# Kernel optimization log

Measured on AMD Instinct MI355X. Metric: run time of the kernel, lower is better.

## Reference

```python
import jax, jax.numpy as jnp
import numpy as np

EPS = 1e-6

def setup_inputs() -> dict:
    key = jax.random.key(0)
    k1, k2, k3 = jax.random.split(key, 3)
    B, N, C = 128, 196, 1024  # B = b*f = 8*16
    x = jax.random.normal(k1, (B, N, C), dtype=jnp.float32)
    w_qkv = jax.random.normal(k2, (3 * C, C), dtype=jnp.float32) * (C ** -0.5)
    w_proj = jax.random.normal(k3, (C, C), dtype=jnp.float32) * (C ** -0.5)
    b_proj = jnp.zeros((C,), dtype=jnp.float32)
    return {"x": x, "w_qkv": w_qkv, "w_proj": w_proj, "b_proj": b_proj, "num_frames": 16}

def reference(x, w_qkv, w_proj, b_proj, num_frames):
    B, N, C = x.shape
    H = 16
    e = C // H
    scale = e ** -0.5
    f = num_frames
    b = B // f
    # qkv projection (no bias), split k-first per rearrange 'b n (k c) -> k b n c'
    qkv = jnp.einsum('bnc,dc->bnd', x, w_qkv)          # [B, N, 3C]
    qkv = qkv.reshape(B, N, 3, H, e)
    q, k, v = qkv[:, :, 0], qkv[:, :, 1], qkv[:, :, 2]  # [B, N, H, e]
    # relu feature map + scale offset
    q_ = jax.nn.relu(q) + scale
    k_ = jax.nn.relu(k) + scale
    # fold frames into the token axis per video: [b, f*n, H, e]
    L = f * N
    q_ = q_.reshape(b, L, H, e)
    k_ = k_.reshape(b, L, H, e)
    v_ = v.reshape(b, L, H, e)
    # linear attention: kv accumulation [b, H, e, e]
    kv = jnp.einsum('bnhe,bnhd->bhed', k_, v_)
    k_sum = jnp.sum(k_, axis=1, keepdims=True)          # [b, 1, H, e]
    z = 1.0 / (jnp.sum(q_ * k_sum, axis=-1) + EPS)       # [b, L, H]
    out = jnp.einsum('bnhe,bhed->bnhd', q_, kv) * z[..., None]  # [b, L, H, e]
    out = out.reshape(B, N, C)
    return jnp.einsum('bnc,dc->bnd', out, w_proj) + b_proj
```

## Files before the change

### kernel.cpp

```cpp
#include <hip/hip_runtime.h>
#include <hip/hip_bf16.h>
#include <stdint.h>

typedef __attribute__((ext_vector_type(8))) short bf16x8;
typedef __attribute__((ext_vector_type(4))) float f32x4;

__device__ __forceinline__ unsigned short f2bf(float f) {
    unsigned u = __builtin_bit_cast(unsigned, f);
    u += 0x7FFF + ((u >> 16) & 1);
    return (unsigned short)(u >> 16);
}
__device__ __forceinline__ float bf2f(unsigned short h) {
    return __builtin_bit_cast(float, (unsigned)h << 16);
}
__device__ __forceinline__ void load_lds16(const void* g, void* l) {
    __builtin_amdgcn_global_load_lds(
        (const __attribute__((address_space(1))) void*)g,
        (__attribute__((address_space(3))) void*)l, 16, 0, 0);
}

__global__ __launch_bounds__(256)
void cvt_kernel(const float* __restrict__ src, unsigned short* __restrict__ dst)
{
    const long i = ((long)blockIdx.x * 256 + threadIdx.x) * 8;
    const float4 a = *(const float4*)(src + i);
    const float4 b = *(const float4*)(src + i + 4);
    bf16x8 r;
    r[0] = (short)f2bf(a.x); r[1] = (short)f2bf(a.y);
    r[2] = (short)f2bf(a.z); r[3] = (short)f2bf(a.w);
    r[4] = (short)f2bf(b.x); r[5] = (short)f2bf(b.y);
    r[6] = (short)f2bf(b.z); r[7] = (short)f2bf(b.w);
    *(bf16x8*)(dst + i) = r;
}

#define LD_A(p, i, s) (*(const bf16x8*)&lds[p][wr][((i) * 16 + fr) * 64 + ((((s) << 2) + qd) ^ cx) * 8])
#define LD_B(p, j, s) (*(const bf16x8*)&lds[p][2 + bh_][(brow_ + (j) * 16 + fr) * 64 + ((((s) << 2) + qd) ^ cx) * 8])

#define LDA4(p, ib) do { \
    afr[0][0] = LD_A(p, (ib)+0, 0); afr[0][1] = LD_A(p, (ib)+0, 1); \
    afr[1][0] = LD_A(p, (ib)+1, 0); afr[1][1] = LD_A(p, (ib)+1, 1); \
    afr[2][0] = LD_A(p, (ib)+2, 0); afr[2][1] = LD_A(p, (ib)+2, 1); \
    afr[3][0] = LD_A(p, (ib)+3, 0); afr[3][1] = LD_A(p, (ib)+3, 1); \
} while (0)

#define LDB2(p, jb) do { \
    bfr[(jb)+0][0] = LD_B(p, (jb)+0, 0); bfr[(jb)+0][1] = LD_B(p, (jb)+0, 1); \
    bfr[(jb)+1][0] = LD_B(p, (jb)+1, 0); bfr[(jb)+1][1] = LD_B(p, (jb)+1, 1); \
} while (0)

#define STAGE_A(p, half, tile) do { \
    const unsigned short* s_ = Ag + (long)((half) * 128) * 1024 + (tile) * 64; \
    unsigned short* d_ = ldsw + ((p) * 4 + (half)) * 8192; \
    load_lds16(s_, d_); \
    load_lds16(s_ + (long)64 * 1024, d_ + 4096); \
} while (0)

#define STAGE_B(p, half, tile) do { \
    const unsigned short* s_ = Bg + (long)((half) * 128) * 1024 + (tile) * 64; \
    unsigned short* d_ = ldsw + ((p) * 4 + 2 + (half)) * 8192; \
    load_lds16(s_, d_); \
    load_lds16(s_ + (long)64 * 1024, d_ + 4096); \
} while (0)

#define MM(ib, jb) do { \
    _Pragma("unroll") \
    for (int i_ = 0; i_ < 4; ++i_) { \
        acc[(ib)+i_][(jb)+0] = __builtin_amdgcn_mfma_f32_16x16x32_bf16(afr[i_][0], bfr[(jb)+0][0], acc[(ib)+i_][(jb)+0], 0, 0, 0); \
        acc[(ib)+i_][(jb)+1] = __builtin_amdgcn_mfma_f32_16x16x32_bf16(afr[i_][0], bfr[(jb)+1][0], acc[(ib)+i_][(jb)+1], 0, 0, 0); \
    } \
    _Pragma("unroll") \
    for (int i_ = 0; i_ < 4; ++i_) { \
        acc[(ib)+i_][(jb)+0] = __builtin_amdgcn_mfma_f32_16x16x32_bf16(afr[i_][1], bfr[(jb)+0][1], acc[(ib)+i_][(jb)+0], 0, 0, 0); \
        acc[(ib)+i_][(jb)+1] = __builtin_amdgcn_mfma_f32_16x16x32_bf16(afr[i_][1], bfr[(jb)+1][1], acc[(ib)+i_][(jb)+1], 0, 0, 0); \
    } \
} while (0)

#define PH_MID() do { \
    __builtin_amdgcn_sched_barrier(0); \
    __builtin_amdgcn_s_barrier(); \
    asm volatile("s_waitcnt lgkmcnt(0)" ::: "memory"); \
    __builtin_amdgcn_sched_barrier(0); \
    __builtin_amdgcn_s_setprio(1); \
} while (0)

#define PH_END() do { \
    __builtin_amdgcn_s_setprio(0); \
    __builtin_amdgcn_s_barrier(); \
} while (0)

#define PH_END_V(n) do { \
    __builtin_amdgcn_s_setprio(0); \
    asm volatile("s_waitcnt vmcnt(" #n ")" ::: "memory"); \
    __builtin_amdgcn_s_barrier(); \
} while (0)

template<int MODE>
__global__ __launch_bounds__(512, 2)
void gemm_bt_kernel(const unsigned short* __restrict__ A,
                    const unsigned short* __restrict__ Bt,
                    __hip_bfloat16* __restrict__ o0,
                    __hip_bfloat16* __restrict__ o1,
                    __hip_bfloat16* __restrict__ o2,
                    float* __restrict__ outf,
                    const float* __restrict__ bias)
{
    constexpr int K  = 1024;
    constexpr int NT = (MODE == 0) ? 12 : 4;
    __shared__ __attribute__((aligned(16))) unsigned short lds[2][4][8192];

    const int bid   = blockIdx.x;
    const int npg   = 8 * NT;
    const int group = bid / npg;
    const int rem   = bid - group * npg;
    const int gm    = (98 - group * 8 < 8) ? (98 - group * 8) : 8;
    const int mt    = group * 8 + rem % gm;
    const int nt    = rem / gm;
    const long m0 = (long)mt * 256;
    const long n0 = (long)nt * 256;

    const int t    = threadIdx.x;
    const int lane = t & 63;
    const int wv   = t >> 6;
    const int wr   = wv >> 2;
    const int wc   = wv & 3;
    const int fr   = lane & 15;
    const int qd   = lane >> 4;
    const int cx   = fr & 7;
    const int bh_   = wc >> 1;
    const int brow_ = (wc & 1) << 6;

    const int srow = t >> 3;
    const int gch  = (t & 7) ^ (srow & 7);
    const unsigned short* Ag = A  + (m0 + srow) * K + gch * 8;
    const unsigned short* Bg = Bt + (n0 + srow) * K + gch * 8;
    unsigned short* const ldsw = &lds[0][0][0] + wv * 512;

    f32x4 acc[8][4] = {};
    bf16x8 afr[4][2], bfr[4][2];

    STAGE_B(0, 0, 0); STAGE_B(0, 1, 0); STAGE_A(0, 0, 0); STAGE_A(0, 1, 0);
    STAGE_B(1, 0, 1); STAGE_B(1, 1, 1);
    asm volatile("s_waitcnt vmcnt(4)" ::: "memory");
    __builtin_amdgcn_s_barrier();

#pragma unroll 1
    for (int it = 0; it < 7; ++it) {
        const int t1 = 2 * it + 1, t2 = 2 * it + 2, t3 = 2 * it + 3;
        LDA4(0, 0); LDB2(0, 0); STAGE_A(1, 0, t1);
        PH_MID(); MM(0, 0); PH_END();
        LDB2(0, 2); STAGE_A(1, 1, t1);
        PH_MID(); MM(0, 2); PH_END();
        LDA4(0, 4); STAGE_B(0, 0, t2);
        PH_MID(); MM(4, 0); PH_END();
        STAGE_B(0, 1, t2);
        PH_MID(); MM(4, 2); PH_END_V(4);
        LDA4(1, 0); LDB2(1, 0); STAGE_A(0, 0, t2);
        PH_MID(); MM(0, 0); PH_END();
        LDB2(1, 2); STAGE_A(0, 1, t2);
        PH_MID(); MM(0, 2); PH_END();
        LDA4(1, 4); STAGE_B(1, 0, t3);
        PH_MID(); MM(4, 0); PH_END();
        STAGE_B(1, 1, t3);
        PH_MID(); MM(4, 2); PH_END_V(4);
    }
    LDA4(0, 0); LDB2(0, 0); STAGE_A(1, 0, 15);
    PH_MID(); MM(0, 0); PH_END();
    LDB2(0, 2); STAGE_A(1, 1, 15);
    PH_MID(); MM(0, 2); PH_END();
    LDA4(0, 4);
    PH_MID(); MM(4, 0); PH_END();
    PH_MID(); MM(4, 2); PH_END_V(0);
    LDA4(1, 0); LDB2(1, 0);
    PH_MID(); MM(0, 0); PH_END();
    LDB2(1, 2);
    PH_MID(); MM(0, 2); PH_END();
    LDA4(1, 4);
    PH_MID(); MM(4, 0); PH_END();
    __builtin_amdgcn_s_barrier();
    asm volatile("s_waitcnt lgkmcnt(0)" ::: "memory");
    __builtin_amdgcn_sched_barrier(0);
    __builtin_amdgcn_s_setprio(1); MM(4, 2); __builtin_amdgcn_s_setprio(0);

    if (MODE == 0) {
        const int which = nt >> 2;
        __hip_bfloat16* dst = (which == 0) ? o0 : (which == 1) ? o1 : o2;
        const int colbase = ((nt & 3) << 8) + wc * 64;
        const bool act = (which < 2);
#pragma unroll
        for (int i = 0; i < 8; ++i) {
            const long mrow = m0 + wr * 128 + i * 16 + qd * 4;
#pragma unroll
            for (int r = 0; r < 4; ++r) {
                const long moff = (mrow + r) * 1024;
#pragma unroll
                for (int j = 0; j < 4; ++j) {
                    float v = acc[i][j][r];
                    if (act) v = fmaxf(v, 0.f) + 0.125f;
                    dst[moff + colbase + j * 16 + fr] = __float2bfloat16(v);
                }
            }
        }
    } else {
        const long nbase = n0 + wc * 64;
#pragma unroll
        for (int i = 0; i < 8; ++i) {
            const long mrow = m0 + wr * 128 + i * 16 + qd * 4;
#pragma unroll
            for (int r = 0; r < 4; ++r) {
                const long moff = (mrow + r) * 1024;
#pragma unroll
                for (int j = 0; j < 4; ++j)
                    outf[moff + nbase + j * 16 + fr] =
                        acc[i][j][r] + bias[nbase + j * 16 + fr];
            }
        }
    }
}

__global__ __launch_bounds__(256)
void kv_partial_kernel(const __hip_bfloat16* __restrict__ kbuf,
                       const __hip_bfloat16* __restrict__ vbuf,
                       float* __restrict__ kvp,
                       float* __restrict__ ksump)
{
    __shared__ float kf[8][512];
    __shared__ float vf[8][512];
    const int t   = threadIdx.x;
    const int bid = blockIdx.x;
    const int sp   = bid % 14;
    const int hoct = (bid / 14) & 1;
    const int bb   = bid / 28;
    const long rowstart = (long)bb * 3136 + sp * 224;

    const int hsub = t >> 5;
    const int w    = t & 31;
    const int E    = w >> 2;
    const int Dq   = w & 3;
    const int cb   = hsub * 64;
    const int e0   = cb + E * 8;
    const int d0   = cb + Dq * 16;

    float kvacc[8][16];
#pragma unroll
    for (int i = 0; i < 8; ++i)
#pragma unroll
        for (int j = 0; j < 16; ++j) kvacc[i][j] = 0.f;
    float ksacc[8] = {0, 0, 0, 0, 0, 0, 0, 0};

    for (int it = 0; it < 28; ++it) {
        __syncthreads();
#pragma unroll
        for (int i = 0; i < 4; ++i) {
            const int idx = t + (i << 8);
            const int rr  = (idx >> 6) & 7;
            const int c   = idx & 63;
            const long grow = rowstart + it * 8 + rr;
            const __hip_bfloat16* srcp =
                ((idx < 512) ? kbuf : vbuf) + grow * 1024 + hoct * 512 + c * 8;
            bf16x8 v8 = *(const bf16x8*)srcp;
            float* dstp = (idx < 512) ? &kf[rr][c * 8] : &vf[rr][c * 8];
#pragma unroll
            for (int jj = 0; jj < 8; ++jj)
                dstp[jj] = bf2f((unsigned short)v8[jj]);
        }
        __syncthreads();
#pragma unroll
        for (int r = 0; r < 8; ++r) {
            float ke[8], vd[16];
#pragma unroll
            for (int i = 0; i < 8; ++i)  ke[i] = kf[r][e0 + i];
#pragma unroll
            for (int j = 0; j < 16; ++j) vd[j] = vf[r][d0 + j];
#pragma unroll
            for (int i = 0; i < 8; ++i) {
                ksacc[i] += ke[i];
#pragma unroll
                for (int j = 0; j < 16; ++j)
                    kvacc[i][j] += ke[i] * vd[j];
            }
        }
    }

    const int bh = bb * 16 + hoct * 8 + hsub;
    const int s2 = E >> 2, qd = E & 3;
    float* outp = kvp + ((long)sp * 128 + bh) * 4096 + ((s2 * 4 + Dq) * 64 + qd * 16) * 8;
#pragma unroll
    for (int fr = 0; fr < 16; ++fr)
#pragma unroll
        for (int jj = 0; jj < 8; ++jj)
            outp[fr * 8 + jj] = kvacc[jj][fr];
    if (Dq == 0) {
#pragma unroll
        for (int i = 0; i < 8; ++i)
            ksump[sp * 8192 + bh * 64 + E * 8 + i] = ksacc[i];
    }
}

__global__ __launch_bounds__(256)
void reduce_kv_kernel(const float* __restrict__ kvp, const float* __restrict__ ksump,
                      unsigned short* __restrict__ kvb, float* __restrict__ ksum)
{
    const int idx = blockIdx.x * 256 + threadIdx.x;
    if (idx < 128 * 4096) {
        float a = 0.f;
#pragma unroll
        for (int s = 0; s < 14; ++s) a += kvp[(long)s * 128 * 4096 + idx];
        kvb[idx] = f2bf(a);
    } else {
        const int j = idx - 128 * 4096;
        if (j < 128 * 64) {
            float a = 0.f;
#pragma unroll
            for (int s = 0; s < 14; ++s) a += ksump[s * 8192 + j];
            ksum[j] = a;
        }
    }
}

__global__ __launch_bounds__(256)
void attn_out_kernel(const __hip_bfloat16* __restrict__ qbuf,
                     const unsigned short* __restrict__ kvb,
                     const float* __restrict__ ksum,
                     __hip_bfloat16* __restrict__ out2)
{
    __shared__ __attribute__((aligned(16))) unsigned short qs[64][64];
    __shared__ float kss[64];
    __shared__ float zs[64];
    const int t   = threadIdx.x;
    const int bid = blockIdx.x;
    const int mc  = bid % 49;
    const int h   = (bid / 49) & 15;
    const int bb  = bid / 784;
    const long bh = bb * 16 + h;
    const long mbase = (long)bb * 3136 + mc * 64;

#pragma unroll
    for (int i = 0; i < 2; ++i) {
        const int idx = t + (i << 8);
        const int row = idx >> 3;
        const int c   = idx & 7;
        *(bf16x8*)&qs[row][c * 8] =
            *(const bf16x8*)(qbuf + (mbase + row) * 1024 + h * 64 + c * 8);
    }
    if (t < 64) kss[t] = ksum[bh * 64 + t];
    __syncthreads();
    if (t < 64) {
        float p = 0.f;
#pragma unroll
        for (int e = 0; e < 64; ++e) p += bf2f(qs[t][e]) * kss[e];
        zs[t] = 1.f / (p + 1e-6f);
    }
    __syncthreads();

    const int lane = t & 63;
    const int wv   = t >> 6;
    const int fr   = lane & 15;
    const int qd   = lane >> 4;

    bf16x8 bfv[2][4];
#pragma unroll
    for (int s2 = 0; s2 < 2; ++s2)
#pragma unroll
        for (int j = 0; j < 4; ++j)
            bfv[s2][j] = *(const bf16x8*)(kvb + bh * 4096 + ((s2 * 4 + j) * 64 + lane) * 8);

    const bf16x8 af0 = *(const bf16x8*)&qs[wv * 16 + fr][qd * 8];
    const bf16x8 af1 = *(const bf16x8*)&qs[wv * 16 + fr][32 + qd * 8];

    float zr[4];
#pragma unroll
    for (int r = 0; r < 4; ++r) zr[r] = zs[wv * 16 + qd * 4 + r];

#pragma unroll
    for (int j = 0; j < 4; ++j) {
        f32x4 acc = {};
        acc = __builtin_amdgcn_mfma_f32_16x16x32_bf16(af0, bfv[0][j], acc, 0, 0, 0);
        acc = __builtin_amdgcn_mfma_f32_16x16x32_bf16(af1, bfv[1][j], acc, 0, 0, 0);
#pragma unroll
        for (int r = 0; r < 4; ++r) {
            const long m = mbase + wv * 16 + qd * 4 + r;
            out2[m * 1024 + h * 64 + j * 16 + fr] = __float2bfloat16(acc[r] * zr[r]);
        }
    }
}

extern "C" void kernel_launch(void* const* d_in, const int* in_sizes, int n_in,
                              void* d_out, int out_size, void* d_ws, size_t ws_size,
                              hipStream_t stream)
{
    const float* x      = (const float*)d_in[0];
    const float* w_qkv  = (const float*)d_in[1];
    const float* w_proj = (const float*)d_in[2];
    const float* b_proj = (const float*)d_in[3];
    float* out = (float*)d_out;

    const long M = 25088;
    char* ws = (char*)d_ws;
    size_t off = 0;
    auto alloc = [&](size_t bytes) {
        char* p = ws + off;
        off += (bytes + 255) & ~(size_t)255;
        return p;
    };
    char* xb_region = alloc(M * 1024 * 2);
    unsigned short* xb     = (unsigned short*)xb_region;
    float*          kvp    = (float*)xb_region;
    float*          ksump  = (float*)(xb_region + (size_t)14 * 128 * 4096 * 4);
    unsigned short* wqkvb  = (unsigned short*)alloc((size_t)3072 * 1024 * 2);
    unsigned short* wprojb = (unsigned short*)alloc((size_t)1024 * 1024 * 2);
    unsigned short* vbuf   = (unsigned short*)alloc(M * 1024 * 2);
    unsigned short* kvb    = (unsigned short*)alloc((size_t)128 * 4096 * 2);
    float*          ksumr  = (float*)alloc((size_t)128 * 64 * 4);
    __hip_bfloat16* qbuf = (__hip_bfloat16*)d_out;
    __hip_bfloat16* kbuf = qbuf + M * 1024;
    __hip_bfloat16* out2 = (__hip_bfloat16*)vbuf;

    cvt_kernel<<<12544, 256, 0, stream>>>(x, xb);
    cvt_kernel<<<1536, 256, 0, stream>>>(w_qkv, wqkvb);
    cvt_kernel<<<512, 256, 0, stream>>>(w_proj, wprojb);
    gemm_bt_kernel<0><<<98 * 12, 512, 0, stream>>>(
        xb, wqkvb, qbuf, kbuf, (__hip_bfloat16*)vbuf, nullptr, nullptr);
    kv_partial_kernel<<<224, 256, 0, stream>>>(kbuf, (const __hip_bfloat16*)vbuf, kvp, ksump);
    reduce_kv_kernel<<<2080, 256, 0, stream>>>(kvp, ksump, kvb, ksumr);
    attn_out_kernel<<<8 * 16 * 49, 256, 0, stream>>>(qbuf, kvb, ksumr, out2);
    gemm_bt_kernel<1><<<98 * 4, 512, 0, stream>>>(
        (const unsigned short*)out2, wprojb, nullptr, nullptr, nullptr, out, b_proj);
}
```

Before: 516.6 us.

## Pre-swizzle LDS layout to fragment order and prefetch fragments a phase ahead

The global-to-LDS staging now writes tiles in MFMA fragment order, so each lane reads its fragment at base + lane*16 with no XOR swizzle arithmetic. The main loop is rescheduled so LDS fragment reads for the next phase are issued before the barrier, overlapping them with the current MFMAs, and the explicit lgkmcnt waits are removed. Both A and B of the next tile are staged up front. The risk is LDS bank conflicts in the new layout, extra register pressure, and hazards from relying on implicit waits for the fragment reads.

```diff
diff --git a/kernel.cpp b/kernel.cpp
--- a/kernel.cpp
+++ b/kernel.cpp
@@ -33,8 +33,8 @@
     *(bf16x8*)(dst + i) = r;
 }
 
-#define LD_A(p, i, s) (*(const bf16x8*)&lds[p][wr][((i) * 16 + fr) * 64 + ((((s) << 2) + qd) ^ cx) * 8])
-#define LD_B(p, j, s) (*(const bf16x8*)&lds[p][2 + bh_][(brow_ + (j) * 16 + fr) * 64 + ((((s) << 2) + qd) ^ cx) * 8])
+#define LD_A(p, i, s) (*(const bf16x8*)(Abase + (p) * 65536 + ((i) * 2 + (s)) * 1024))
+#define LD_B(p, j, s) (*(const bf16x8*)(Bbase + (p) * 65536 + ((j) * 2 + (s)) * 1024))
 
 #define LDA4(p, ib) do { \
     afr[0][0] = LD_A(p, (ib)+0, 0); afr[0][1] = LD_A(p, (ib)+0, 1); \
@@ -49,17 +49,17 @@
 } while (0)
 
 #define STAGE_A(p, half, tile) do { \
-    const unsigned short* s_ = Ag + (long)((half) * 128) * 1024 + (tile) * 64; \
+    const unsigned short* s_ = Ag + (long)(half) * 131072 + (tile) * 64; \
     unsigned short* d_ = ldsw + ((p) * 4 + (half)) * 8192; \
     load_lds16(s_, d_); \
-    load_lds16(s_ + (long)64 * 1024, d_ + 4096); \
+    load_lds16(s_ + 65536, d_ + 4096); \
 } while (0)
 
 #define STAGE_B(p, half, tile) do { \
-    const unsigned short* s_ = Bg + (long)((half) * 128) * 1024 + (tile) * 64; \
+    const unsigned short* s_ = Bg + (long)(half) * 131072 + (tile) * 64; \
     unsigned short* d_ = ldsw + ((p) * 4 + 2 + (half)) * 8192; \
     load_lds16(s_, d_); \
-    load_lds16(s_ + (long)64 * 1024, d_ + 4096); \
+    load_lds16(s_ + 65536, d_ + 4096); \
 } while (0)
 
 #define MM(ib, jb) do { \
@@ -75,24 +75,18 @@
     } \
 } while (0)
 
-#define PH_MID() do { \
+#define MID() do { \
     __builtin_amdgcn_sched_barrier(0); \
     __builtin_amdgcn_s_barrier(); \
-    asm volatile("s_waitcnt lgkmcnt(0)" ::: "memory"); \
     __builtin_amdgcn_sched_barrier(0); \
     __builtin_amdgcn_s_setprio(1); \
 } while (0)
-
-#define PH_END() do { \
-    __builtin_amdgcn_s_setprio(0); \
+#define SP0() __builtin_amdgcn_s_setprio(0)
+#define BARR() do { \
+    __builtin_amdgcn_sched_barrier(0); \
     __builtin_amdgcn_s_barrier(); \
 } while (0)
-
-#define PH_END_V(n) do { \
-    __builtin_amdgcn_s_setprio(0); \
-    asm volatile("s_waitcnt vmcnt(" #n ")" ::: "memory"); \
-    __builtin_amdgcn_s_barrier(); \
-} while (0)
+#define VM(n) asm volatile("s_waitcnt vmcnt(" #n ")" ::: "memory")
 
 template<int MODE>
 __global__ __launch_bounds__(512, 2)
@@ -125,61 +119,48 @@
     const int wc   = wv & 3;
     const int fr   = lane & 15;
     const int qd   = lane >> 4;
-    const int cx   = fr & 7;
-    const int bh_   = wc >> 1;
-    const int brow_ = (wc & 1) << 6;
-
-    const int srow = t >> 3;
-    const int gch  = (t & 7) ^ (srow & 7);
-    const unsigned short* Ag = A  + (m0 + srow) * K + gch * 8;
-    const unsigned short* Bg = Bt + (n0 + srow) * K + gch * 8;
+    const int bh_  = wc >> 1;
+
+    const char* Abase = (const char*)&lds[0][wr][0] + lane * 16;
+    const char* Bbase = (const char*)&lds[0][2 + bh_][0] + (wc & 1) * 8192 + lane * 16;
+
+    const int srow = ((t >> 7) << 4) + (t & 15);
+    const int kcol = ((t >> 6) & 1) * 32 + ((t >> 4) & 3) * 8;
+    const unsigned short* Ag = A  + (m0 + srow) * K + kcol;
+    const unsigned short* Bg = Bt + (n0 + srow) * K + kcol;
     unsigned short* const ldsw = &lds[0][0][0] + wv * 512;
 
     f32x4 acc[8][4] = {};
     bf16x8 afr[4][2], bfr[4][2];
 
     STAGE_B(0, 0, 0); STAGE_B(0, 1, 0); STAGE_A(0, 0, 0); STAGE_A(0, 1, 0);
-    STAGE_B(1, 0, 1); STAGE_B(1, 1, 1);
-    asm volatile("s_waitcnt vmcnt(4)" ::: "memory");
-    __builtin_amdgcn_s_barrier();
+    STAGE_B(1, 0, 1); STAGE_B(1, 1, 1); STAGE_A(1, 0, 1); STAGE_A(1, 1, 1);
+    VM(8);
+    BARR();
+    LDB2(0, 0); LDA4(0, 0); LDB2(0, 2);
 
 #pragma unroll 1
     for (int it = 0; it < 7; ++it) {
-        const int t1 = 2 * it + 1, t2 = 2 * it + 2, t3 = 2 * it + 3;
-        LDA4(0, 0); LDB2(0, 0); STAGE_A(1, 0, t1);
-        PH_MID(); MM(0, 0); PH_END();
-        LDB2(0, 2); STAGE_A(1, 1, t1);
-        PH_MID(); MM(0, 2); PH_END();
-        LDA4(0, 4); STAGE_B(0, 0, t2);
-        PH_MID(); MM(4, 0); PH_END();
-        STAGE_B(0, 1, t2);
-        PH_MID(); MM(4, 2); PH_END_V(4);
-        LDA4(1, 0); LDB2(1, 0); STAGE_A(0, 0, t2);
-        PH_MID(); MM(0, 0); PH_END();
-        LDB2(1, 2); STAGE_A(0, 1, t2);
-        PH_MID(); MM(0, 2); PH_END();
-        LDA4(1, 4); STAGE_B(1, 0, t3);
-        PH_MID(); MM(4, 0); PH_END();
-        STAGE_B(1, 1, t3);
-        PH_MID(); MM(4, 2); PH_END_V(4);
-    }
-    LDA4(0, 0); LDB2(0, 0); STAGE_A(1, 0, 15);
-    PH_MID(); MM(0, 0); PH_END();
-    LDB2(0, 2); STAGE_A(1, 1, 15);
-    PH_MID(); MM(0, 2); PH_END();
-    LDA4(0, 4);
-    PH_MID(); MM(4, 0); PH_END();
-    PH_MID(); MM(4, 2); PH_END_V(0);
-    LDA4(1, 0); LDB2(1, 0);
-    PH_MID(); MM(0, 0); PH_END();
-    LDB2(1, 2);
-    PH_MID(); MM(0, 2); PH_END();
-    LDA4(1, 4);
-    PH_MID(); MM(4, 0); PH_END();
-    __builtin_amdgcn_s_barrier();
-    asm volatile("s_waitcnt lgkmcnt(0)" ::: "memory");
-    __builtin_amdgcn_sched_barrier(0);
-    __builtin_amdgcn_s_setprio(1); MM(4, 2); __builtin_amdgcn_s_setprio(0);
+        const int t2 = 2 * it + 2, t3 = 2 * it + 3;
+        STAGE_B(0, 0, t2); MID(); MM(0, 0); SP0(); BARR();
+        STAGE_B(0, 1, t2); MID(); MM(0, 2); SP0(); LDA4(0, 4); BARR();
+        STAGE_A(0, 0, t2); MID(); MM(4, 0); SP0(); VM(6); BARR();
+        STAGE_A(0, 1, t2); MID(); MM(4, 2); SP0();
+        LDB2(1, 0); LDA4(1, 0); LDB2(1, 2); BARR();
+        STAGE_B(1, 0, t3); MID(); MM(0, 0); SP0(); BARR();
+        STAGE_B(1, 1, t3); MID(); MM(0, 2); SP0(); LDA4(1, 4); BARR();
+        STAGE_A(1, 0, t3); MID(); MM(4, 0); SP0(); VM(6); BARR();
+        STAGE_A(1, 1, t3); MID(); MM(4, 2); SP0();
+        LDB2(0, 0); LDA4(0, 0); LDB2(0, 2); BARR();
+    }
+    __builtin_amdgcn_s_setprio(1); MM(0, 0); SP0(); BARR();
+    __builtin_amdgcn_s_setprio(1); MM(0, 2); SP0(); LDA4(0, 4); BARR();
+    __builtin_amdgcn_s_setprio(1); MM(4, 0); SP0(); VM(0); BARR();
+    __builtin_amdgcn_s_setprio(1); MM(4, 2); SP0();
+    LDB2(1, 0); LDA4(1, 0); LDB2(1, 2); BARR();
+    __builtin_amdgcn_s_setprio(1); MM(0, 0); SP0(); BARR();
+    __builtin_amdgcn_s_setprio(1); MM(0, 2); SP0(); LDA4(1, 4); BARR();
+    __builtin_amdgcn_s_setprio(1); MM(4, 0); MM(4, 2); SP0();
 
     if (MODE == 0) {
         const int which = nt >> 2;
```

Result: slower. 560.8 us (+8.5%).
